# Performance work log

Measured on AMD Instinct MI355X. Metric: run time of the kernel, lower is better.

Reference implementation:

```python
import jax, jax.numpy as jnp
import numpy as np

N_NODES = 100000
N_EDGES = 1600000
IN_C = 128
HID_C = 32
HEADS = 4
OUT_C = 40
N_GRAPHS = 64
NEG_SLOPE = 0.2  # PyG GATConv default


def setup_inputs() -> dict:
    key = jax.random.key(0)
    ks = jax.random.split(key, 12)
    x = jax.random.normal(ks[0], (N_NODES, IN_C), dtype=jnp.float32)
    edge_index = jax.random.randint(ks[1], (2, N_EDGES), 0, N_NODES, dtype=jnp.int64)
    batch = jnp.sort(jax.random.randint(ks[2], (N_NODES,), 0, N_GRAPHS, dtype=jnp.int64))
    s1 = 1.0 / np.sqrt(IN_C)
    s2 = 1.0 / np.sqrt(HEADS * HID_C)
    W1 = jax.random.normal(ks[3], (IN_C, HEADS * HID_C), dtype=jnp.float32) * s1
    a1_src = jax.random.normal(ks[4], (HEADS, HID_C), dtype=jnp.float32) * s1
    a1_dst = jax.random.normal(ks[5], (HEADS, HID_C), dtype=jnp.float32) * s1
    b1 = jnp.zeros((HEADS * HID_C,), dtype=jnp.float32)
    W2 = jax.random.normal(ks[6], (HEADS * HID_C, OUT_C), dtype=jnp.float32) * s2
    a2_src = jax.random.normal(ks[7], (1, OUT_C), dtype=jnp.float32) * s2
    a2_dst = jax.random.normal(ks[8], (1, OUT_C), dtype=jnp.float32) * s2
    b2 = jnp.zeros((OUT_C,), dtype=jnp.float32)
    return {"x": x, "edge_index": edge_index, "batch": batch,
            "W1": W1, "a1_src": a1_src, "a1_dst": a1_dst, "b1": b1,
            "W2": W2, "a2_src": a2_src, "a2_dst": a2_dst, "b2": b2}


def gat_conv(x, src, dst, W, a_src, a_dst, bias, heads, out_c, concat):
    """PyG-style GATConv (eval mode, self-loops included in src/dst)."""
    N = x.shape[0]
    h = (x @ W).reshape(N, heads, out_c)              # [N,H,C]
    alpha_s = jnp.einsum('nhc,hc->nh', h, a_src)      # [N,H]
    alpha_d = jnp.einsum('nhc,hc->nh', h, a_dst)
    e = alpha_s[src] + alpha_d[dst]                   # [E,H]
    e = jnp.where(e > 0, e, NEG_SLOPE * e)            # LeakyReLU(0.2)
    # segment softmax over edges grouped by destination node
    m = jax.ops.segment_max(e, dst, num_segments=N)   # [N,H]
    ex = jnp.exp(e - m[dst])
    denom = jax.ops.segment_sum(ex, dst, num_segments=N)
    alpha = ex / (denom[dst] + 1e-16)                 # [E,H]
    msg = h[src] * alpha[..., None]                   # [E,H,C]
    out = jax.ops.segment_sum(msg, dst, num_segments=N)  # [N,H,C]
    if concat:
        out = out.reshape(N, heads * out_c)
    else:
        out = out.mean(axis=1)
    return out + bias


def reference(x, edge_index, batch, W1, a1_src, a1_dst, b1, W2, a2_src, a2_dst, b2):
    N = x.shape[0]
    # add self-loops (PyG GATConv default add_self_loops=True)
    loop = jnp.arange(N, dtype=edge_index.dtype)
    src = jnp.concatenate([edge_index[0], loop])
    dst = jnp.concatenate([edge_index[1], loop])
    h = gat_conv(x, src, dst, W1, a1_src, a1_dst, b1, HEADS, HID_C, concat=True)
    h = jax.nn.elu(h)
    h = gat_conv(h, src, dst, W2, a2_src, a2_dst, b2, 1, OUT_C, concat=False)
    # global mean pool over graphs
    sums = jax.ops.segment_sum(h, batch, num_segments=N_GRAPHS)
    counts = jax.ops.segment_sum(jnp.ones((N,), dtype=h.dtype), batch, num_segments=N_GRAPHS)
    return sums / jnp.maximum(counts, 1.0)[:, None]
```

## Files before the change

### kernel.cpp

```cpp
#include <hip/hip_runtime.h>

#define NNODES 100000
#define NEDGES 1600000
#define ETOT   1700000
#define NGRAPH 64
#define NEG    0.2f
#define NB_SCAN 98
#define NPART  8
#define DPP    12500
#define SCAT_BPP 128
#define SCAT_CHR 12500
#define DSL    98
#define PCH    1024
#define NHB    1563
#define NGB    1563
#define CSTR   16

using f32x2 = __attribute__((ext_vector_type(2))) float;

__device__ __forceinline__ float f4get(const float4& v, int j) {
    return j == 0 ? v.x : j == 1 ? v.y : j == 2 ? v.z : v.w;
}

__device__ __forceinline__ unsigned short f2bf(float f) {
    unsigned u = __float_as_uint(f);
    u = (u + 0x7fffu + ((u >> 16) & 1u)) >> 16;
    return (unsigned short)u;
}
__device__ __forceinline__ float bf_lo(unsigned u) { return __uint_as_float(u << 16); }
__device__ __forceinline__ float bf_hi(unsigned u) { return __uint_as_float(u & 0xffff0000u); }

__global__ __launch_bounds__(256) void k_init(int* __restrict__ cnt, float* __restrict__ partial) {
    int t = threadIdx.x, b = blockIdx.x;
#pragma unroll
    for (int j = 0; j < 4; ++j) {
        int idx = b * 1024 + t * 4 + j;
        if (idx < NNODES) cnt[(size_t)idx * CSTR] = 1;
    }
    int pi = b * 256 + t;
    if (pi < NGRAPH * 40) partial[pi] = 0.f;
}

__global__ __launch_bounds__(256, 4) void k_fused1(const int* __restrict__ ei,
        int* __restrict__ cnt, int* __restrict__ rank,
        const float* __restrict__ x, const float* __restrict__ W1,
        const float* __restrict__ a1s, const float* __restrict__ a1d,
        unsigned* __restrict__ h1q, float* __restrict__ as1, float* __restrict__ ad1) {
    __shared__ float sX[64 * 128];
    int bid = blockIdx.x;
    if (bid & 1) {
        int hb = bid >> 1;
        int base = hb * 1024 + threadIdx.x;
        int e0 = base, e1 = base + 256, e2 = base + 512, e3 = base + 768;
        bool v0 = e0 < NEDGES, v1 = e1 < NEDGES, v2 = e2 < NEDGES, v3 = e3 < NEDGES;
        int d0 = 0, d1 = 0, d2 = 0, d3 = 0;
        if (v0) d0 = ei[NEDGES + e0];
        if (v1) d1 = ei[NEDGES + e1];
        if (v2) d2 = ei[NEDGES + e2];
        if (v3) d3 = ei[NEDGES + e3];
        int r0 = 0, r1 = 0, r2 = 0, r3 = 0;
        if (v0) r0 = atomicAdd(&cnt[(size_t)d0 * CSTR], 1);
        if (v1) r1 = atomicAdd(&cnt[(size_t)d1 * CSTR], 1);
        if (v2) r2 = atomicAdd(&cnt[(size_t)d2 * CSTR], 1);
        if (v3) r3 = atomicAdd(&cnt[(size_t)d3 * CSTR], 1);
        if (v0) rank[e0] = r0;
        if (v1) rank[e1] = r1;
        if (v2) rank[e2] = r2;
        if (v3) rank[e3] = r3;
        return;
    }
    int gb = bid >> 1;
    if (gb >= NGB) return;
    int t = threadIdx.x;
    int nbase = gb * 64;
    int nrows = NNODES - nbase; if (nrows > 64) nrows = 64;
    {
        const float4* X4 = (const float4*)(x + (size_t)nbase * 128);
        float4* sX4 = (float4*)sX;
        for (int i = t; i < nrows * 32; i += 256) sX4[i] = X4[i];
    }
    __syncthreads();

    int colg = t & 31, rowg = t >> 5;
    int c0 = colg * 4, n0 = rowg * 8;
    float acc[8][4];
#pragma unroll
    for (int i = 0; i < 8; ++i)
        acc[i][0] = acc[i][1] = acc[i][2] = acc[i][3] = 0.f;

    for (int k = 0; k < 128; k += 4) {
        float4 w0 = *(const float4*)&W1[(size_t)(k + 0) * 128 + c0];
        float4 w1 = *(const float4*)&W1[(size_t)(k + 1) * 128 + c0];
        float4 w2 = *(const float4*)&W1[(size_t)(k + 2) * 128 + c0];
        float4 w3 = *(const float4*)&W1[(size_t)(k + 3) * 128 + c0];
#pragma unroll
        for (int i = 0; i < 8; ++i) {
            float4 xv = *(const float4*)&sX[(n0 + i) * 128 + k];
            acc[i][0] = fmaf(xv.x, w0.x, acc[i][0]); acc[i][1] = fmaf(xv.x, w0.y, acc[i][1]);
            acc[i][2] = fmaf(xv.x, w0.z, acc[i][2]); acc[i][3] = fmaf(xv.x, w0.w, acc[i][3]);
            acc[i][0] = fmaf(xv.y, w1.x, acc[i][0]); acc[i][1] = fmaf(xv.y, w1.y, acc[i][1]);
            acc[i][2] = fmaf(xv.y, w1.z, acc[i][2]); acc[i][3] = fmaf(xv.y, w1.w, acc[i][3]);
            acc[i][0] = fmaf(xv.z, w2.x, acc[i][0]); acc[i][1] = fmaf(xv.z, w2.y, acc[i][1]);
            acc[i][2] = fmaf(xv.z, w2.z, acc[i][2]); acc[i][3] = fmaf(xv.z, w2.w, acc[i][3]);
            acc[i][0] = fmaf(xv.w, w3.x, acc[i][0]); acc[i][1] = fmaf(xv.w, w3.y, acc[i][1]);
            acc[i][2] = fmaf(xv.w, w3.z, acc[i][2]); acc[i][3] = fmaf(xv.w, w3.w, acc[i][3]);
        }
    }

    int head = colg >> 3;
    float ws0 = a1s[c0], ws1 = a1s[c0 + 1], ws2 = a1s[c0 + 2], ws3 = a1s[c0 + 3];
    float wd0 = a1d[c0], wd1 = a1d[c0 + 1], wd2 = a1d[c0 + 2], wd3 = a1d[c0 + 3];
#pragma unroll
    for (int i = 0; i < 8; ++i) {
        int n = n0 + i;
        float ps = acc[i][0] * ws0 + acc[i][1] * ws1 + acc[i][2] * ws2 + acc[i][3] * ws3;
        float pd = acc[i][0] * wd0 + acc[i][1] * wd1 + acc[i][2] * wd2 + acc[i][3] * wd3;
        ps += __shfl_xor(ps, 1); ps += __shfl_xor(ps, 2); ps += __shfl_xor(ps, 4);
        pd += __shfl_xor(pd, 1); pd += __shfl_xor(pd, 2); pd += __shfl_xor(pd, 4);
        if (n < nrows) {
            int q = __builtin_amdgcn_cvt_pk_fp8_f32(acc[i][0], acc[i][1], 0, false);
            q = __builtin_amdgcn_cvt_pk_fp8_f32(acc[i][2], acc[i][3], q, true);
            h1q[((size_t)(nbase + n)) * 32 + colg] = (unsigned)q;
            if ((colg & 7) == 0) {
                as1[(size_t)(nbase + n) * 4 + head] = ps;
                ad1[(size_t)(nbase + n) * 4 + head] = pd;
            }
        }
    }
}

__global__ __launch_bounds__(256) void k_scan1(const int* __restrict__ cnt,
                                               int* __restrict__ excl,
                                               int* __restrict__ bsum) {
    __shared__ int tmp[256];
    int t = threadIdx.x;
    int base = blockIdx.x * 1024 + t * 4;
    int v0 = base + 0 < NNODES ? cnt[(size_t)(base + 0) * CSTR] : 0;
    int v1 = base + 1 < NNODES ? cnt[(size_t)(base + 1) * CSTR] : 0;
    int v2 = base + 2 < NNODES ? cnt[(size_t)(base + 2) * CSTR] : 0;
    int v3 = base + 3 < NNODES ? cnt[(size_t)(base + 3) * CSTR] : 0;
    int tot = v0 + v1 + v2 + v3;
    tmp[t] = tot;
    __syncthreads();
    for (int off = 1; off < 256; off <<= 1) {
        int x = (t >= off) ? tmp[t - off] : 0;
        __syncthreads();
        tmp[t] += x;
        __syncthreads();
    }
    int tbase = tmp[t] - tot;
    if (base + 0 < NNODES) excl[base + 0] = tbase;
    if (base + 1 < NNODES) excl[base + 1] = tbase + v0;
    if (base + 2 < NNODES) excl[base + 2] = tbase + v0 + v1;
    if (base + 3 < NNODES) excl[base + 3] = tbase + v0 + v1 + v2;
    if (t == 255) bsum[blockIdx.x] = tmp[255];
}

__global__ __launch_bounds__(256) void k_offs(const int* __restrict__ excl,
                                              const int* __restrict__ bsum,
                                              int* __restrict__ offs) {
    __shared__ int sp;
    int b = blockIdx.x, t = threadIdx.x;
    if (t == 0) {
        int p = 0;
        for (int i = 0; i < b; ++i) p += bsum[i];
        sp = p;
    }
    __syncthreads();
    int prefix = sp;
#pragma unroll
    for (int j = 0; j < 4; ++j) {
        int idx = b * 1024 + t * 4 + j;
        if (idx < NNODES) offs[idx] = excl[idx] + prefix;
    }
}

__global__ __launch_bounds__(256) void k_scatter(const int* __restrict__ ei,
                                                 const int* __restrict__ rank,
                                                 const int* __restrict__ offs,
                                                 int* __restrict__ csr_src) {
    int p = blockIdx.x & (NPART - 1);
    int chunk = blockIdx.x / NPART;
    int dlo = p * DPP, dhi = dlo + DPP;
    {
        int d = dlo + chunk * DSL + threadIdx.x;
        if (threadIdx.x < DSL && d < dhi) csr_src[offs[d]] = d;
    }
    int e0 = chunk * SCAT_CHR;
    int e1 = e0 + SCAT_CHR; if (e1 > NEDGES) e1 = NEDGES;
    for (int e = e0 + threadIdx.x; e < e1; e += 1024) {
        int eA = e, eB = e + 256, eC = e + 512, eD = e + 768;
        bool vA = eA < e1, vB = eB < e1, vC = eC < e1, vD = eD < e1;
        int dA = -1, dB = -1, dC = -1, dD = -1;
        if (vA) dA = ei[NEDGES + eA];
        if (vB) dB = ei[NEDGES + eB];
        if (vC) dC = ei[NEDGES + eC];
        if (vD) dD = ei[NEDGES + eD];
        if (dA >= dlo && dA < dhi) csr_src[offs[dA] + rank[eA]] = ei[eA];
        if (dB >= dlo && dB < dhi) csr_src[offs[dB] + rank[eB]] = ei[eB];
        if (dC >= dlo && dC < dhi) csr_src[offs[dC] + rank[eC]] = ei[eC];
        if (dD >= dlo && dD < dhi) csr_src[offs[dD] + rank[eD]] = ei[eD];
    }
}

__global__ __launch_bounds__(256) void k_node1(const int* __restrict__ csr_src,
        const int* __restrict__ offs, const int* __restrict__ cnt,
        const unsigned* __restrict__ h1q,
        const float4* __restrict__ as1v, const float4* __restrict__ ad1v,
        unsigned* __restrict__ out1b) {
    __shared__ float4 exbuf[8][32];
    int t = threadIdx.x;
    int grp = t >> 5, lane = t & 31;
    int node = blockIdx.x * 8 + grp;
    if (node >= NNODES) return;
    int head = lane >> 3;
    int off = offs[node];
    int deg = cnt[(size_t)node * CSTR];
    float4 adv = ad1v[node];
    float4 dp = make_float4(0.f, 0.f, 0.f, 0.f);
    float4 acc = make_float4(0.f, 0.f, 0.f, 0.f);
    const float* exs = (const float*)&exbuf[grp][0];

    for (int base = 0; base < deg; base += 32) {
        int m = deg - base; if (m > 32) m = 32;
        int sv = 0;
        if (lane < m) {
            sv = csr_src[off + base + lane];
            float4 av = as1v[sv];
            float v; float4 e;
            v = av.x + adv.x; v = v > 0.f ? v : NEG * v; e.x = __expf(v);
            v = av.y + adv.y; v = v > 0.f ? v : NEG * v; e.y = __expf(v);
            v = av.z + adv.z; v = v > 0.f ? v : NEG * v; e.z = __expf(v);
            v = av.w + adv.w; v = v > 0.f ? v : NEG * v; e.w = __expf(v);
            exbuf[grp][lane] = e;
            dp.x += e.x; dp.y += e.y; dp.z += e.z; dp.w += e.w;
        }
        __builtin_amdgcn_wave_barrier();
        int i = 0;
        for (; i + 4 <= m; i += 4) {
            int s0 = __shfl(sv, i + 0, 32);
            int s1 = __shfl(sv, i + 1, 32);
            int s2 = __shfl(sv, i + 2, 32);
            int s3 = __shfl(sv, i + 3, 32);
            unsigned q0 = h1q[(size_t)s0 * 32 + lane];
            unsigned q1 = h1q[(size_t)s1 * 32 + lane];
            unsigned q2 = h1q[(size_t)s2 * 32 + lane];
            unsigned q3 = h1q[(size_t)s3 * 32 + lane];
            float a0 = exs[(i + 0) * 4 + head];
            float a1 = exs[(i + 1) * 4 + head];
            float a2 = exs[(i + 2) * 4 + head];
            float a3 = exs[(i + 3) * 4 + head];
            f32x2 lo, hi;
            lo = __builtin_amdgcn_cvt_pk_f32_fp8((int)q0, false);
            hi = __builtin_amdgcn_cvt_pk_f32_fp8((int)q0, true);
            acc.x = fmaf(lo.x, a0, acc.x); acc.y = fmaf(lo.y, a0, acc.y);
            acc.z = fmaf(hi.x, a0, acc.z); acc.w = fmaf(hi.y, a0, acc.w);
            lo = __builtin_amdgcn_cvt_pk_f32_fp8((int)q1, false);
            hi = __builtin_amdgcn_cvt_pk_f32_fp8((int)q1, true);
            acc.x = fmaf(lo.x, a1, acc.x); acc.y = fmaf(lo.y, a1, acc.y);
            acc.z = fmaf(hi.x, a1, acc.z); acc.w = fmaf(hi.y, a1, acc.w);
            lo = __builtin_amdgcn_cvt_pk_f32_fp8((int)q2, false);
            hi = __builtin_amdgcn_cvt_pk_f32_fp8((int)q2, true);
            acc.x = fmaf(lo.x, a2, acc.x); acc.y = fmaf(lo.y, a2, acc.y);
            acc.z = fmaf(hi.x, a2, acc.z); acc.w = fmaf(hi.y, a2, acc.w);
            lo = __builtin_amdgcn_cvt_pk_f32_fp8((int)q3, false);
            hi = __builtin_amdgcn_cvt_pk_f32_fp8((int)q3, true);
            acc.x = fmaf(lo.x, a3, acc.x); acc.y = fmaf(lo.y, a3, acc.y);
            acc.z = fmaf(hi.x, a3, acc.z); acc.w = fmaf(hi.y, a3, acc.w);
        }
        for (; i < m; ++i) {
            int s = __shfl(sv, i, 32);
            float a = exs[i * 4 + head];
            unsigned hq = h1q[(size_t)s * 32 + lane];
            f32x2 lo = __builtin_amdgcn_cvt_pk_f32_fp8((int)hq, false);
            f32x2 hi = __builtin_amdgcn_cvt_pk_f32_fp8((int)hq, true);
            acc.x = fmaf(lo.x, a, acc.x);
            acc.y = fmaf(lo.y, a, acc.y);
            acc.z = fmaf(hi.x, a, acc.z);
            acc.w = fmaf(hi.y, a, acc.w);
        }
        __builtin_amdgcn_wave_barrier();
    }
#pragma unroll
    for (int msk = 1; msk < 32; msk <<= 1) {
        dp.x += __shfl_xor(dp.x, msk, 32);
        dp.y += __shfl_xor(dp.y, msk, 32);
        dp.z += __shfl_xor(dp.z, msk, 32);
        dp.w += __shfl_xor(dp.w, msk, 32);
    }
    float inv = 1.f / f4get(dp, head);
    unsigned p0 = (unsigned)f2bf(acc.x * inv) | ((unsigned)f2bf(acc.y * inv) << 16);
    unsigned p1 = (unsigned)f2bf(acc.z * inv) | ((unsigned)f2bf(acc.w * inv) << 16);
    uint2 pk; pk.x = p0; pk.y = p1;
    *(uint2*)&out1b[(size_t)node * 64 + lane * 2] = pk;
}

__global__ __launch_bounds__(256) void k_gemm2(const unsigned* __restrict__ in_b,
                                               const float* __restrict__ W2,
                                               const float* __restrict__ b1,
                                               const float* __restrict__ a2s,
                                               const float* __restrict__ a2d,
                                               unsigned short* __restrict__ h2b,
                                               float* __restrict__ as2,
                                               float* __restrict__ ad2) {
    __shared__ float sW[128 * 40];
    __shared__ float sX[128 * 132];
    int t = threadIdx.x;
    for (int i = t; i < 128 * 40 / 4; i += 256) ((float4*)sW)[i] = ((const float4*)W2)[i];
    int nbase = blockIdx.x * 128;
    int nrows = NNODES - nbase; if (nrows > 128) nrows = 128;
    {
        const uint4* X4 = (const uint4*)(in_b + (size_t)nbase * 64);
        for (int i = t; i < nrows * 16; i += 256) {
            int row = i >> 4, c8 = i & 15;
            uint4 v = X4[i];
            float4 bb0 = *(const float4*)&b1[c8 * 8];
            float4 bb1 = *(const float4*)&b1[c8 * 8 + 4];
            float f0 = bf_lo(v.x) + bb0.x, f1 = bf_hi(v.x) + bb0.y;
            float f2 = bf_lo(v.y) + bb0.z, f3 = bf_hi(v.y) + bb0.w;
            float f4 = bf_lo(v.z) + bb1.x, f5 = bf_hi(v.z) + bb1.y;
            float f6 = bf_lo(v.w) + bb1.z, f7 = bf_hi(v.w) + bb1.w;
            f0 = f0 > 0.f ? f0 : __expf(f0) - 1.f;
            f1 = f1 > 0.f ? f1 : __expf(f1) - 1.f;
            f2 = f2 > 0.f ? f2 : __expf(f2) - 1.f;
            f3 = f3 > 0.f ? f3 : __expf(f3) - 1.f;
            f4 = f4 > 0.f ? f4 : __expf(f4) - 1.f;
            f5 = f5 > 0.f ? f5 : __expf(f5) - 1.f;
            f6 = f6 > 0.f ? f6 : __expf(f6) - 1.f;
            f7 = f7 > 0.f ? f7 : __expf(f7) - 1.f;
            float* sp = &sX[row * 132 + c8 * 8];
            *(float4*)sp       = make_float4(f0, f1, f2, f3);
            *(float4*)(sp + 4) = make_float4(f4, f5, f6, f7);
        }
    }
    __syncthreads();

    int colg = t & 7, nodeg = t >> 3;
    int c0 = colg * 5;
    float acc[4][5];
#pragma unroll
    for (int i = 0; i < 4; ++i)
#pragma unroll
        for (int c = 0; c < 5; ++c) acc[i][c] = 0.f;

    for (int k = 0; k < 128; k += 4) {
        float4 xv[4];
#pragma unroll
        for (int i = 0; i < 4; ++i)
            xv[i] = *(const float4*)&sX[(nodeg + 32 * i) * 132 + k];
#pragma unroll
        for (int j = 0; j < 4; ++j) {
            float w0 = sW[(k + j) * 40 + c0 + 0];
            float w1 = sW[(k + j) * 40 + c0 + 1];
            float w2 = sW[(k + j) * 40 + c0 + 2];
            float w3 = sW[(k + j) * 40 + c0 + 3];
            float w4 = sW[(k + j) * 40 + c0 + 4];
#pragma unroll
            for (int i = 0; i < 4; ++i) {
                float xs = f4get(xv[i], j);
                acc[i][0] = fmaf(xs, w0, acc[i][0]);
                acc[i][1] = fmaf(xs, w1, acc[i][1]);
                acc[i][2] = fmaf(xs, w2, acc[i][2]);
                acc[i][3] = fmaf(xs, w3, acc[i][3]);
                acc[i][4] = fmaf(xs, w4, acc[i][4]);
            }
        }
    }

    float ws0 = a2s[c0], ws1 = a2s[c0 + 1], ws2 = a2s[c0 + 2], ws3 = a2s[c0 + 3], ws4 = a2s[c0 + 4];
    float wd0 = a2d[c0], wd1 = a2d[c0 + 1], wd2 = a2d[c0 + 2], wd3 = a2d[c0 + 3], wd4 = a2d[c0 + 4];
#pragma unroll
    for (int i = 0; i < 4; ++i) {
        int n = nodeg + 32 * i;
        float ps = acc[i][0]*ws0 + acc[i][1]*ws1 + acc[i][2]*ws2 + acc[i][3]*ws3 + acc[i][4]*ws4;
        float pd = acc[i][0]*wd0 + acc[i][1]*wd1 + acc[i][2]*wd2 + acc[i][3]*wd3 + acc[i][4]*wd4;
        ps += __shfl_xor(ps, 1); ps += __shfl_xor(ps, 2); ps += __shfl_xor(ps, 4);
        pd += __shfl_xor(pd, 1); pd += __shfl_xor(pd, 2); pd += __shfl_xor(pd, 4);
        if (n < nrows) {
            unsigned short* hp = h2b + (size_t)(nbase + n) * 40 + c0;
#pragma unroll
            for (int c = 0; c < 5; ++c) hp[c] = f2bf(acc[i][c]);
            if (colg == 0) {
                as2[nbase + n] = ps;
                ad2[nbase + n] = pd;
            }
        }
    }
}

__global__ __launch_bounds__(256) void k_node2(const int* __restrict__ csr_src,
        const int* __restrict__ offs, const int* __restrict__ cnt,
        const unsigned short* __restrict__ h2b,
        const float* __restrict__ as2, const float* __restrict__ ad2,
        float* __restrict__ out2) {
    int t = threadIdx.x;
    int grp = t >> 4, lane = t & 15;
    int node = blockIdx.x * 16 + grp;
    if (node >= NNODES) return;
    int off = offs[node];
    int deg = cnt[(size_t)node * CSTR];
    float adv = ad2[node];
    float dp = 0.f;
    float4 acc = make_float4(0.f, 0.f, 0.f, 0.f);

    for (int base = 0; base < deg; base += 16) {
        int m = deg - base; if (m > 16) m = 16;
        int sv = 0; float ex = 0.f;
        if (lane < m) {
            sv = csr_src[off + base + lane];
            float v = as2[sv] + adv;
            v = v > 0.f ? v : NEG * v;
            ex = __expf(v);
            dp += ex;
        }
        int i = 0;
        for (; i + 4 <= m; i += 4) {
            int s0 = __shfl(sv, i + 0, 16);
            int s1 = __shfl(sv, i + 1, 16);
            int s2 = __shfl(sv, i + 2, 16);
            int s3 = __shfl(sv, i + 3, 16);
            float a0 = __shfl(ex, i + 0, 16);
            float a1 = __shfl(ex, i + 1, 16);
            float a2 = __shfl(ex, i + 2, 16);
            float a3 = __shfl(ex, i + 3, 16);
            if (lane < 10) {
                uint2 h0 = *(const uint2*)(h2b + (size_t)s0 * 40 + lane * 4);
                uint2 h1 = *(const uint2*)(h2b + (size_t)s1 * 40 + lane * 4);
                uint2 h2 = *(const uint2*)(h2b + (size_t)s2 * 40 + lane * 4);
                uint2 h3 = *(const uint2*)(h2b + (size_t)s3 * 40 + lane * 4);
                acc.x = fmaf(bf_lo(h0.x), a0, acc.x); acc.y = fmaf(bf_hi(h0.x), a0, acc.y);
                acc.z = fmaf(bf_lo(h0.y), a0, acc.z); acc.w = fmaf(bf_hi(h0.y), a0, acc.w);
                acc.x = fmaf(bf_lo(h1.x), a1, acc.x); acc.y = fmaf(bf_hi(h1.x), a1, acc.y);
                acc.z = fmaf(bf_lo(h1.y), a1, acc.z); acc.w = fmaf(bf_hi(h1.y), a1, acc.w);
                acc.x = fmaf(bf_lo(h2.x), a2, acc.x); acc.y = fmaf(bf_hi(h2.x), a2, acc.y);
                acc.z = fmaf(bf_lo(h2.y), a2, acc.z); acc.w = fmaf(bf_hi(h2.y), a2, acc.w);
                acc.x = fmaf(bf_lo(h3.x), a3, acc.x); acc.y = fmaf(bf_hi(h3.x), a3, acc.y);
                acc.z = fmaf(bf_lo(h3.y), a3, acc.z); acc.w = fmaf(bf_hi(h3.y), a3, acc.w);
            }
        }
        for (; i < m; ++i) {
            int s = __shfl(sv, i, 16);
            float a = __shfl(ex, i, 16);
            if (lane < 10) {
                uint2 hv = *(const uint2*)(h2b + (size_t)s * 40 + lane * 4);
                acc.x = fmaf(bf_lo(hv.x), a, acc.x);
                acc.y = fmaf(bf_hi(hv.x), a, acc.y);
                acc.z = fmaf(bf_lo(hv.y), a, acc.z);
                acc.w = fmaf(bf_hi(hv.y), a, acc.w);
            }
        }
    }
#pragma unroll
    for (int msk = 1; msk < 16; msk <<= 1) dp += __shfl_xor(dp, msk, 16);
    float inv = 1.f / dp;
    if (lane < 10) {
        float4 o; o.x = acc.x * inv; o.y = acc.y * inv; o.z = acc.z * inv; o.w = acc.w * inv;
        *(float4*)(out2 + (size_t)node * 40 + lane * 4) = o;
    }
}

__global__ __launch_bounds__(256) void k_pool1(const float* __restrict__ out2,
        const int* __restrict__ batch, float* __restrict__ partial) {
    int t = threadIdx.x;
    if (t >= 240) return;
    int r = t / 40, c = t - r * 40;
    int base = blockIdx.x * PCH;
    int end = base + PCH; if (end > NNODES) end = NNODES;
    float sum = 0.f; int gcur = -1;
    for (int n = base + r; n < end; n += 6) {
        int g = batch[n];
        if (g != gcur) {
            if (gcur >= 0) unsafeAtomicAdd(&partial[gcur * 40 + c], sum);
            gcur = g; sum = 0.f;
        }
        sum += out2[(size_t)n * 40 + c];
    }
    if (gcur >= 0) unsafeAtomicAdd(&partial[gcur * 40 + c], sum);
}

__global__ void k_pool2(const float* __restrict__ partial, const int* __restrict__ batch,
                        const float* __restrict__ b2, float* __restrict__ out) {
    int i = blockIdx.x * 256 + threadIdx.x;
    if (i >= NGRAPH * 40) return;
    int g = i / 40, c = i - g * 40;
    int lo, hi;
    { int a = 0, b = NNODES; while (a < b) { int m = (a + b) >> 1; if (batch[m] < g) a = m + 1; else b = m; } lo = a; }
    { int a = lo, b = NNODES; while (a < b) { int m = (a + b) >> 1; if (batch[m] < g + 1) a = m + 1; else b = m; } hi = a; }
    int cntg = hi - lo;
    out[i] = cntg > 0 ? partial[i] / (float)cntg + b2[c] : 0.f;
}

extern "C" void kernel_launch(void* const* d_in, const int* in_sizes, int n_in,
                              void* d_out, int out_size, void* d_ws, size_t ws_size,
                              hipStream_t stream) {
    const float* x    = (const float*)d_in[0];
    const int*   ei   = (const int*)d_in[1];
    const int*   batch= (const int*)d_in[2];
    const float* W1   = (const float*)d_in[3];
    const float* a1s  = (const float*)d_in[4];
    const float* a1d  = (const float*)d_in[5];
    const float* b1   = (const float*)d_in[6];
    const float* W2   = (const float*)d_in[7];
    const float* a2s  = (const float*)d_in[8];
    const float* a2d  = (const float*)d_in[9];
    const float* b2   = (const float*)d_in[10];
    float* out = (float*)d_out;

    int* cnt      = (int*)d_ws;
    float* partial= (float*)(cnt + (size_t)NNODES * CSTR);
    int* excl     = (int*)(partial + NGRAPH * 40);
    int* offs     = excl + NNODES;
    int* bsum     = offs + NNODES;
    int* rank     = bsum + 128;
    int* csr      = rank + NEDGES;
    float* as1    = (float*)(csr + ETOT);
    float* ad1    = as1 + (size_t)NNODES * 4;
    unsigned* h1q = (unsigned*)(ad1 + (size_t)NNODES * 4);
    unsigned* out1b = h1q + (size_t)NNODES * 32;
    float* as2    = (float*)(out1b + (size_t)NNODES * 64);
    float* ad2    = as2 + NNODES;
    unsigned short* h2b = (unsigned short*)(ad2 + NNODES);
    float* out2   = (float*)(h2b + (size_t)NNODES * 40);

    k_init<<<NB_SCAN, 256, 0, stream>>>(cnt, partial);

    k_fused1<<<2 * NHB, 256, 0, stream>>>(ei, cnt, rank, x, W1, a1s, a1d, h1q, as1, ad1);

    k_scan1<<<NB_SCAN, 256, 0, stream>>>(cnt, excl, bsum);
    k_offs<<<NB_SCAN, 256, 0, stream>>>(excl, bsum, offs);
    k_scatter<<<NPART * SCAT_BPP, 256, 0, stream>>>(ei, rank, offs, csr);

    k_node1<<<(NNODES + 7) / 8, 256, 0, stream>>>(csr, offs, cnt, h1q,
                                                  (const float4*)as1, (const float4*)ad1, out1b);

    k_gemm2<<<(NNODES + 127) / 128, 256, 0, stream>>>(out1b, W2, b1, a2s, a2d, h2b, as2, ad2);
    k_node2<<<(NNODES + 15) / 16, 256, 0, stream>>>(csr, offs, cnt, h2b, as2, ad2, out2);

    k_pool1<<<(NNODES + PCH - 1) / PCH, 256, 0, stream>>>(out2, batch, partial);
    k_pool2<<<(NGRAPH * 40 + 255) / 256, 256, 0, stream>>>(partial, batch, b2, out);
}
```

Measured before the change: 346.8 us.

## Pack degree counters densely and rebalance histogram vs GEMM blocks in fused kernel

Removes the 16-int stride padding on the per-node degree counter array, so counters are contiguous and scan/node kernels read them with coalesced loads. The fused kernel now gives one histogram block for every three GEMM blocks, and each histogram block processes 3072 edges in a loop instead of 1024 edges. Denser counters may raise atomic contention on shared cache lines, which the padding was presumably avoiding, while improving read locality in the downstream kernels.

```diff
diff --git a/kernel.cpp b/kernel.cpp
--- a/kernel.cpp
+++ b/kernel.cpp
@@ -12,9 +12,10 @@
 #define SCAT_CHR 12500
 #define DSL    98
 #define PCH    1024
-#define NHB    1563
 #define NGB    1563
-#define CSTR   16
+#define HB     521
+#define HEPB   3072
+#define FGRID  2084
 
 using f32x2 = __attribute__((ext_vector_type(2))) float;
 
@@ -35,7 +36,7 @@
 #pragma unroll
     for (int j = 0; j < 4; ++j) {
         int idx = b * 1024 + t * 4 + j;
-        if (idx < NNODES) cnt[(size_t)idx * CSTR] = 1;
+        if (idx < NNODES) cnt[idx] = 1;
     }
     int pi = b * 256 + t;
     if (pi < NGRAPH * 40) partial[pi] = 0.f;
@@ -48,28 +49,32 @@
         unsigned* __restrict__ h1q, float* __restrict__ as1, float* __restrict__ ad1) {
     __shared__ float sX[64 * 128];
     int bid = blockIdx.x;
-    if (bid & 1) {
-        int hb = bid >> 1;
-        int base = hb * 1024 + threadIdx.x;
-        int e0 = base, e1 = base + 256, e2 = base + 512, e3 = base + 768;
-        bool v0 = e0 < NEDGES, v1 = e1 < NEDGES, v2 = e2 < NEDGES, v3 = e3 < NEDGES;
-        int d0 = 0, d1 = 0, d2 = 0, d3 = 0;
-        if (v0) d0 = ei[NEDGES + e0];
-        if (v1) d1 = ei[NEDGES + e1];
-        if (v2) d2 = ei[NEDGES + e2];
-        if (v3) d3 = ei[NEDGES + e3];
-        int r0 = 0, r1 = 0, r2 = 0, r3 = 0;
-        if (v0) r0 = atomicAdd(&cnt[(size_t)d0 * CSTR], 1);
-        if (v1) r1 = atomicAdd(&cnt[(size_t)d1 * CSTR], 1);
-        if (v2) r2 = atomicAdd(&cnt[(size_t)d2 * CSTR], 1);
-        if (v3) r3 = atomicAdd(&cnt[(size_t)d3 * CSTR], 1);
-        if (v0) rank[e0] = r0;
-        if (v1) rank[e1] = r1;
-        if (v2) rank[e2] = r2;
-        if (v3) rank[e3] = r3;
+    if ((bid & 3) == 3) {
+        int hb = bid >> 2;
+        int t = threadIdx.x;
+        int e0 = hb * HEPB;
+        int e1 = e0 + HEPB; if (e1 > NEDGES) e1 = NEDGES;
+        for (int e = e0 + t; e < e1; e += 1024) {
+            int eA = e, eB = e + 256, eC = e + 512, eD = e + 768;
+            bool vA = eA < e1, vB = eB < e1, vC = eC < e1, vD = eD < e1;
+            int dA = 0, dB = 0, dC = 0, dD = 0;
+            if (vA) dA = ei[NEDGES + eA];
+            if (vB) dB = ei[NEDGES + eB];
+            if (vC) dC = ei[NEDGES + eC];
+            if (vD) dD = ei[NEDGES + eD];
+            int rA = 0, rB = 0, rC = 0, rD = 0;
+            if (vA) rA = atomicAdd(&cnt[dA], 1);
+            if (vB) rB = atomicAdd(&cnt[dB], 1);
+            if (vC) rC = atomicAdd(&cnt[dC], 1);
+            if (vD) rD = atomicAdd(&cnt[dD], 1);
+            if (vA) rank[eA] = rA;
+            if (vB) rank[eB] = rB;
+            if (vC) rank[eC] = rC;
+            if (vD) rank[eD] = rD;
+        }
         return;
     }
-    int gb = bid >> 1;
+    int gb = (bid >> 2) * 3 + (bid & 3);
     if (gb >= NGB) return;
     int t = threadIdx.x;
     int nbase = gb * 64;
@@ -135,10 +140,10 @@
     __shared__ int tmp[256];
     int t = threadIdx.x;
     int base = blockIdx.x * 1024 + t * 4;
-    int v0 = base + 0 < NNODES ? cnt[(size_t)(base + 0) * CSTR] : 0;
-    int v1 = base + 1 < NNODES ? cnt[(size_t)(base + 1) * CSTR] : 0;
-    int v2 = base + 2 < NNODES ? cnt[(size_t)(base + 2) * CSTR] : 0;
-    int v3 = base + 3 < NNODES ? cnt[(size_t)(base + 3) * CSTR] : 0;
+    int v0 = base + 0 < NNODES ? cnt[base + 0] : 0;
+    int v1 = base + 1 < NNODES ? cnt[base + 1] : 0;
+    int v2 = base + 2 < NNODES ? cnt[base + 2] : 0;
+    int v3 = base + 3 < NNODES ? cnt[base + 3] : 0;
     int tot = v0 + v1 + v2 + v3;
     tmp[t] = tot;
     __syncthreads();
@@ -215,7 +220,7 @@
     if (node >= NNODES) return;
     int head = lane >> 3;
     int off = offs[node];
-    int deg = cnt[(size_t)node * CSTR];
+    int deg = cnt[node];
     float4 adv = ad1v[node];
     float4 dp = make_float4(0.f, 0.f, 0.f, 0.f);
     float4 acc = make_float4(0.f, 0.f, 0.f, 0.f);
@@ -398,7 +403,7 @@
     int node = blockIdx.x * 16 + grp;
     if (node >= NNODES) return;
     int off = offs[node];
-    int deg = cnt[(size_t)node * CSTR];
+    int deg = cnt[node];
     float adv = ad2[node];
     float dp = 0.f;
     float4 acc = make_float4(0.f, 0.f, 0.f, 0.f);
@@ -507,7 +512,7 @@
     float* out = (float*)d_out;
 
     int* cnt      = (int*)d_ws;
-    float* partial= (float*)(cnt + (size_t)NNODES * CSTR);
+    float* partial= (float*)(cnt + NNODES);
     int* excl     = (int*)(partial + NGRAPH * 40);
     int* offs     = excl + NNODES;
     int* bsum     = offs + NNODES;
@@ -524,7 +529,7 @@
 
     k_init<<<NB_SCAN, 256, 0, stream>>>(cnt, partial);
 
-    k_fused1<<<2 * NHB, 256, 0, stream>>>(ei, cnt, rank, x, W1, a1s, a1d, h1q, as1, ad1);
+    k_fused1<<<FGRID, 256, 0, stream>>>(ei, cnt, rank, x, W1, a1s, a1d, h1q, as1, ad1);
 
     k_scan1<<<NB_SCAN, 256, 0, stream>>>(cnt, excl, bsum);
     k_offs<<<NB_SCAN, 256, 0, stream>>>(excl, bsum, offs);
```

After: 331.9 us, median of 2. 4.3% less time.
